# Optimization experiments

Measured on AMD Instinct MI355X. Metric: run time of the kernel, lower is better.

Reference implementation:

```python
import jax, jax.numpy as jnp
import numpy as np

B, L, D_IN, D, P, NL = 8, 4096, 64, 512, 512, 3
EPS = 1e-5


def _ln(x, w, b):
    m = x.mean(-1, keepdims=True)
    v = ((x - m) ** 2).mean(-1, keepdims=True)
    return (x - m) * jax.lax.rsqrt(v + EPS) * w + b


def _gelu(x):
    return jax.nn.gelu(x, approximate=False)  # torch default = exact erf GELU


def _s5_scan(u, lam_re, lam_im, Bre, Bim, Cre, Cim, Dp, log_step):
    # u: (L, D). Diagonal complex SSM with ZOH discretization.
    lam = lam_re + 1j * lam_im                      # (P,)
    step = jnp.exp(log_step)                        # (P,)
    lam_bar = jnp.exp(lam * step)                   # (P,)
    Bt = Bre + 1j * Bim                             # (P, D)
    B_bar = ((lam_bar - 1.0) / lam)[:, None] * Bt   # (P, D)
    Bu = u.astype(jnp.complex64) @ B_bar.T          # (L, P)
    A = jnp.broadcast_to(lam_bar, Bu.shape)         # (L, P)

    def binop(a, b):
        A1, b1 = a
        A2, b2 = b
        return (A2 * A1, A2 * b1 + b2)

    _, xs = jax.lax.associative_scan(binop, (A, Bu))  # (L, P) states
    Ct = Cre + 1j * Cim                               # (D, P)
    return 2.0 * jnp.real(xs @ Ct.T) + Dp * u          # (L, D)


def setup_inputs() -> dict:
    key = jax.random.key(0)
    ks = iter(jax.random.split(key, 32))
    r = lambda s, sc=1.0: sc * jax.random.normal(next(ks), s, dtype=jnp.float32)
    inp = {}
    inp['x'] = r((B, L, D_IN))
    inp['lengths'] = jax.random.randint(next(ks), (B,), 1, L + 1, dtype=jnp.int32)
    inp['enc_w'] = r((D_IN, D), 0.05)
    inp['enc_b'] = jnp.zeros((D,), jnp.float32)
    # S5 SSM params per layer (stacked over NL)
    inp['lam_re'] = -jnp.exp(r((NL, P), 0.5))          # stable: Re(Lambda) < 0
    inp['lam_im'] = np.pi * r((NL, P))
    inp['Bre'] = r((NL, P, D), 1.0 / np.sqrt(D))
    inp['Bim'] = r((NL, P, D), 1.0 / np.sqrt(D))
    inp['Cre'] = r((NL, D, P), 1.0 / np.sqrt(P))
    inp['Cim'] = r((NL, D, P), 1.0 / np.sqrt(P))
    inp['Dp'] = r((NL, D))
    inp['log_step'] = jax.random.uniform(next(ks), (NL, P), jnp.float32, np.log(1e-3), np.log(1e-1))
    # S5Block norms and GEGLU FFN (ff_enc: D->2D no bias, ff_dec: D->D no bias)
    inp['an_w'] = jnp.ones((NL, D), jnp.float32)
    inp['an_b'] = jnp.zeros((NL, D), jnp.float32)
    inp['fn_w'] = jnp.ones((NL, D), jnp.float32)
    inp['fn_b'] = jnp.zeros((NL, D), jnp.float32)
    inp['ffe_w'] = r((NL, 2 * D, D), 1.0 / np.sqrt(D))
    inp['ffd_w'] = r((NL, D, D), 1.0 / np.sqrt(D))
    # outer prenorm LayerNorms
    inp['norm_w'] = jnp.ones((NL, D), jnp.float32)
    inp['norm_b'] = jnp.zeros((NL, D), jnp.float32)
    inp['head_w'] = r((1, D), 0.05)
    inp['head_b'] = jnp.zeros((1,), jnp.float32)
    return inp


def reference(x, lengths, enc_w, enc_b, lam_re, lam_im, Bre, Bim, Cre, Cim, Dp,
              log_step, an_w, an_b, fn_w, fn_b, ffe_w, ffd_w, norm_w, norm_b,
              head_w, head_b):
    h = x @ enc_w + enc_b  # (B, L, D)
    s5_b = jax.vmap(_s5_scan, in_axes=(0, None, None, None, None, None, None, None, None))
    for i in range(NL):
        z = _ln(h, norm_w[i], norm_b[i])  # prenorm (dropout = identity in eval)
        # --- S5Block ---
        fx = _ln(z, an_w[i], an_b[i])
        z = _gelu(s5_b(fx, lam_re[i], lam_im[i], Bre[i], Bim[i], Cre[i], Cim[i], Dp[i], log_step[i])) + fx
        fx = _ln(z, fn_w[i], fn_b[i])
        e = fx @ ffe_w[i].T                      # (B, L, 2D)
        a, g = jnp.split(e, 2, axis=-1)
        z = (a * _gelu(g)) @ ffd_w[i].T + fx      # GEGLU + residual
        h = h + z
    mask = (jnp.arange(L)[None, :] < lengths[:, None])[..., None]  # (B, L, 1)
    pooled = (h * mask).sum(axis=1) / jnp.maximum(lengths, 1)[:, None].astype(h.dtype)
    return (pooled @ head_w.T + head_b).squeeze(-1)  # (B,)
```

## Files before the change

kernel.cpp:

```cpp
#include <hip/hip_runtime.h>
#include <hip/hip_bf16.h>
#include <stdint.h>

#define BB 8
#define LL 4096
#define D_IN 64
#define DD 512
#define PP 512
#define NL 3
#define MTOK (BB * LL)
#define SCHUNK 64
#define SCHUNK_LOG 6
#define NCHUNK (LL / SCHUNK)
#define NCHUNK_LOG 6

typedef __bf16 bf16x8 __attribute__((ext_vector_type(8)));
typedef __bf16 bf16x4 __attribute__((ext_vector_type(4)));
typedef float f32x4 __attribute__((ext_vector_type(4)));

typedef const __attribute__((address_space(1))) void gvoid_t;
typedef __attribute__((address_space(3))) void svoid_t;

__device__ __forceinline__ void async16(const __bf16* g, __bf16* l) {
    __builtin_amdgcn_global_load_lds((gvoid_t*)g, (svoid_t*)l, 16, 0, 0);
}

__device__ __forceinline__ float gelu_f(float x) {
    return 0.5f * x * (1.0f + erff(x * 0.70710678118654752440f));
}
__device__ __forceinline__ float wred(float v) {
#pragma unroll
    for (int o = 32; o > 0; o >>= 1) v += __shfl_xor(v, o, 64);
    return v;
}
__device__ __forceinline__ float bflo(uint32_t u) { return __builtin_bit_cast(float, (uint32_t)(u << 16)); }
__device__ __forceinline__ float bfhi(uint32_t u) { return __builtin_bit_cast(float, (uint32_t)(u & 0xffff0000u)); }
__device__ __forceinline__ uint32_t packbf2(float a, float b) {
    unsigned short ha = __builtin_bit_cast(unsigned short, (__bf16)a);
    unsigned short hb = __builtin_bit_cast(unsigned short, (__bf16)b);
    return (uint32_t)ha | ((uint32_t)hb << 16);
}
__device__ __forceinline__ float ldf(const void* p, long i, int f) {
    return f ? ((const float*)p)[i] : (float)((const __bf16*)p)[i];
}
__device__ __forceinline__ void split1(float v, __bf16& h, __bf16& l) {
    h = (__bf16)v;
    l = (__bf16)(v - (float)h);
}

__global__ void detect(const uint32_t* __restrict__ an_w_raw, int* __restrict__ flag) {
    if (threadIdx.x == 0) *flag = (an_w_raw[0] == 0x3F800000u) ? 1 : 0;
}

template <bool AL, bool BL>
__device__ __forceinline__ void gemm_kloop(
    const __bf16* __restrict__ Ah, const __bf16* __restrict__ Al,
    const __bf16* __restrict__ Bh, const __bf16* __restrict__ Bl,
    long ga, long gb, int lda, int K,
    __bf16* dAh, __bf16* dAl, __bf16* dBh, __bf16* dBl,
    const __bf16* sAh, const __bf16* sAl, const __bf16* sBh, const __bf16* sBl,
    int wm, int wn, int fr, int co, f32x4 (&acc)[4][4])
{
    constexpr int HB = 16384;

    auto stage = [&](int boff, int k0) {
        async16(Ah + ga + k0, dAh + boff);
        async16(Ah + ga + k0 + 16 * (long)lda, dAh + boff + 512);
        if constexpr (AL) {
            async16(Al + ga + k0, dAl + boff);
            async16(Al + ga + k0 + 16 * (long)lda, dAl + boff + 512);
        }
        async16(Bh + gb + k0, dBh + boff);
        async16(Bh + gb + k0 + 16 * (long)K, dBh + boff + 512);
        if constexpr (BL) {
            async16(Bl + gb + k0, dBl + boff);
            async16(Bl + gb + k0 + 16 * (long)K, dBl + boff + 512);
        }
    };

    stage(0, 0);
    asm volatile("s_waitcnt vmcnt(0)" ::: "memory");
    __builtin_amdgcn_s_barrier();
    __builtin_amdgcn_sched_barrier(0);

    int roff = 0;
    for (int k0 = 0; k0 < K; k0 += 32) {
        if (k0 + 32 < K) stage(roff ^ HB, k0 + 32);

        bf16x8 afh[4], afl[4], bfh[4], bfl[4];
#pragma unroll
        for (int i = 0; i < 4; i++) {
            afh[i] = *(const bf16x8*)(sAh + roff + (wm * 64 + i * 16 + fr) * 32 + co);
            bfh[i] = *(const bf16x8*)(sBh + roff + (wn * 64 + i * 16 + fr) * 32 + co);
            if constexpr (AL) afl[i] = *(const bf16x8*)(sAl + roff + (wm * 64 + i * 16 + fr) * 32 + co);
            if constexpr (BL) bfl[i] = *(const bf16x8*)(sBl + roff + (wn * 64 + i * 16 + fr) * 32 + co);
        }
#pragma unroll
        for (int i = 0; i < 4; i++)
#pragma unroll
            for (int j = 0; j < 4; j++) {
                if constexpr (BL)
                    acc[i][j] = __builtin_amdgcn_mfma_f32_16x16x32_bf16(afh[i], bfl[j], acc[i][j], 0, 0, 0);
                if constexpr (AL)
                    acc[i][j] = __builtin_amdgcn_mfma_f32_16x16x32_bf16(afl[i], bfh[j], acc[i][j], 0, 0, 0);
                acc[i][j] = __builtin_amdgcn_mfma_f32_16x16x32_bf16(afh[i], bfh[j], acc[i][j], 0, 0, 0);
            }

        asm volatile("s_waitcnt vmcnt(0) lgkmcnt(0)" ::: "memory");
        __builtin_amdgcn_s_barrier();
        __builtin_amdgcn_sched_barrier(0);
        roff ^= HB;
    }
}

template <int MODE, bool ARAW, bool BRAW>
__global__ __launch_bounds__(256) void gemm_bt(
    const __bf16* __restrict__ Ah, const __bf16* __restrict__ Al, int lda,
    const __bf16* __restrict__ Bh, const __bf16* __restrict__ Bl,
    int M, int N, int K,
    __bf16* outh, __bf16* outl, float* h32,
    __bf16* fxh, __bf16* fxl, const float* __restrict__ vec,
    const int* __restrict__ lengths, float* __restrict__ partials, int b0,
    const int* __restrict__ flag)
{
    __shared__ __attribute__((aligned(16))) char smem[65536];
    __bf16* sAh = (__bf16*)smem;
    __bf16* sAl = (__bf16*)(smem + 8192);
    __bf16* sBh = (__bf16*)(smem + 16384);
    __bf16* sBl = (__bf16*)(smem + 24576);

    const int tid = threadIdx.x;
    const int lane = tid & 63;
    const int wave = tid >> 6;
    const int wm = wave & 1, wn = wave >> 1;
    const long m0 = (long)blockIdx.x * 128;
    const long n0 = (long)blockIdx.y * 128;

    f32x4 acc[4][4] = {};

    const int sr = lane >> 2;
    const int sc = ((lane & 3) ^ ((sr >> 1) & 3)) * 8;
    const long ga = (m0 + wave * 32 + sr) * (long)lda + sc;
    const long gb = (n0 + wave * 32 + sr) * (long)K + sc;
    __bf16* dAh = sAh + wave * 1024;
    __bf16* dAl = sAl + wave * 1024;
    __bf16* dBh = sBh + wave * 1024;
    __bf16* dBl = sBl + wave * 1024;

    const int fr = lane & 15;
    const int co = ((lane >> 4) ^ ((fr >> 1) & 3)) * 8;

    if constexpr (!ARAW && !BRAW) {
        gemm_kloop<true, true>(Ah, Al, Bh, Bl, ga, gb, lda, K, dAh, dAl, dBh, dBl,
                               sAh, sAl, sBh, sBl, wm, wn, fr, co, acc);
    } else {
        const int f32ds = *flag;
        if (f32ds) {
            gemm_kloop<true, true>(Ah, Al, Bh, Bl, ga, gb, lda, K, dAh, dAl, dBh, dBl,
                                   sAh, sAl, sBh, sBl, wm, wn, fr, co, acc);
        } else if constexpr (ARAW && BRAW) {
            gemm_kloop<false, false>(Ah, Al, Bh, Bl, ga, gb, lda, K, dAh, dAl, dBh, dBl,
                                     sAh, sAl, sBh, sBl, wm, wn, fr, co, acc);
        } else if constexpr (!ARAW && BRAW) {
            gemm_kloop<true, false>(Ah, Al, Bh, Bl, ga, gb, lda, K, dAh, dAl, dBh, dBl,
                                    sAh, sAl, sBh, sBl, wm, wn, fr, co, acc);
        } else {
            gemm_kloop<false, true>(Ah, Al, Bh, Bl, ga, gb, lda, K, dAh, dAl, dBh, dBl,
                                    sAh, sAl, sBh, sBl, wm, wn, fr, co, acc);
        }
    }

    float* scratch = (float*)smem + wave * 1088;
    const int er = (lane >> 4) * 4;
    const int ec = lane & 15;
    const int lr_rd = lane >> 3;
    const int lc_rd = (lane & 7) * 8;

    float pacc = 0.f;
    int lenb = 0;
    if (MODE == 5) lenb = lengths[b0 + (int)(blockIdx.x >> 5)];

#pragma unroll
    for (int i = 0; i < 4; i++) {
#pragma unroll
        for (int j = 0; j < 4; j++)
#pragma unroll
            for (int r = 0; r < 4; r++)
                scratch[(er + r) * 68 + j * 16 + ec] = acc[i][j][r];
#pragma unroll
        for (int s = 0; s < 2; s++) {
            const int lr = s * 8 + lr_rd;
            float v8[8];
            *(f32x4*)v8       = *(const f32x4*)&scratch[lr * 68 + lc_rd];
            *(f32x4*)(v8 + 4) = *(const f32x4*)&scratch[lr * 68 + lc_rd + 4];
            const long gm = m0 + wm * 64 + i * 16 + lr;
            const int gc = (int)n0 + wn * 64 + lc_rd;
            if (MODE == 0) {
                const long idx = gm * N + gc;
                bf16x8 h8, l8;
#pragma unroll
                for (int e = 0; e < 8; e++) { __bf16 h, l; split1(v8[e], h, l); h8[e] = h; l8[e] = l; }
                *(bf16x8*)(outh + idx) = h8;
                *(bf16x8*)(outl + idx) = l8;
            } else if (MODE == 1) {
                const long idx = gm * N + gc;
                f32x4 o0, o1;
#pragma unroll
                for (int e = 0; e < 4; e++) { o0[e] = v8[e] + vec[gc + e]; o1[e] = v8[4 + e] + vec[gc + 4 + e]; }
                *(f32x4*)(h32 + idx) = o0;
                *(f32x4*)(h32 + idx + 4) = o1;
            } else if (MODE == 2) {
                const long idx = gm * N + gc;
                const bf16x8 uh = *(const bf16x8*)(fxh + idx);
                const bf16x8 ul = *(const bf16x8*)(fxl + idx);
                bf16x8 h8, l8;
#pragma unroll
                for (int e = 0; e < 8; e++) {
                    const float u = (float)uh[e] + (float)ul[e];
                    const float z = gelu_f(v8[e] + vec[gc + e] * u) + u;
                    __bf16 h, l; split1(z, h, l); h8[e] = h; l8[e] = l;
                }
                *(bf16x8*)(fxh + idx) = h8;
                *(bf16x8*)(fxl + idx) = l8;
            } else if (MODE == 3 || MODE == 5) {
                const long idx = gm * N + gc;
                const bf16x8 uh = *(const bf16x8*)(fxh + idx);
                const bf16x8 ul = *(const bf16x8*)(fxl + idx);
                f32x4 o0 = *(const f32x4*)(h32 + idx);
                f32x4 o1 = *(const f32x4*)(h32 + idx + 4);
#pragma unroll
                for (int e = 0; e < 4; e++) {
                    o0[e] += v8[e] + (float)uh[e] + (float)ul[e];
                    o1[e] += v8[4 + e] + (float)uh[4 + e] + (float)ul[4 + e];
                }
                if (MODE == 3) {
                    *(f32x4*)(h32 + idx) = o0;
                    *(f32x4*)(h32 + idx + 4) = o1;
                } else {
                    if ((int)(gm & (LL - 1)) < lenb) {
#pragma unroll
                        for (int e = 0; e < 4; e++)
                            pacc += o0[e] * vec[gc + e] + o1[e] * vec[gc + 4 + e];
                    }
                }
            } else {
                const long tidx = gm * (N / 2) + (gc >> 1);
                bf16x4 h4, l4;
#pragma unroll
                for (int q = 0; q < 4; q++) {
                    const float t = v8[2 * q] * gelu_f(v8[2 * q + 1]);
                    __bf16 h, l; split1(t, h, l); h4[q] = h; l4[q] = l;
                }
                *(bf16x4*)(outh + tidx) = h4;
                *(bf16x4*)(outl + tidx) = l4;
            }
        }
    }

    if (MODE == 5) {
        pacc = wred(pacc);
        float* red = (float*)(smem + 17408);
        if (lane == 0) red[wave] = pacc;
        __syncthreads();
        if (tid == 0)
            partials[(long)(b0 + (int)(blockIdx.x >> 5)) * 128 +
                     (int)(blockIdx.x & 31) * 4 + (int)blockIdx.y] =
                red[0] + red[1] + red[2] + red[3];
    }
}

template <bool DBL, bool F32IN>
__global__ __launch_bounds__(256) void ln_kernel(
    const float* __restrict__ xf, const __bf16* xh, const __bf16* xl,
    __bf16* oh, __bf16* ol,
    const float* __restrict__ w1, const float* __restrict__ b1,
    const float* __restrict__ w2, const float* __restrict__ b2)
{
    const int lane = threadIdx.x & 63;
    const int wave = threadIdx.x >> 6;
    const long row = (long)blockIdx.x * 4 + wave;
    const int c0 = lane * 8;

    float v[8];
    if (F32IN) {
        const float* xp = xf + row * DD + c0;
        const float4 a = *(const float4*)xp;
        const float4 b = *(const float4*)(xp + 4);
        v[0] = a.x; v[1] = a.y; v[2] = a.z; v[3] = a.w;
        v[4] = b.x; v[5] = b.y; v[6] = b.z; v[7] = b.w;
    } else {
        const bf16x8 a = *(const bf16x8*)(xh + row * DD + c0);
        const bf16x8 b = *(const bf16x8*)(xl + row * DD + c0);
#pragma unroll
        for (int j = 0; j < 8; j++) v[j] = (float)a[j] + (float)b[j];
    }

    float s = 0.f;
#pragma unroll
    for (int j = 0; j < 8; j++) s += v[j];
    s = wred(s);
    float m = s * (1.0f / DD);
    float q = 0.f;
#pragma unroll
    for (int j = 0; j < 8; j++) { const float d = v[j] - m; q += d * d; }
    q = wred(q);
    float rstd = rsqrtf(q * (1.0f / DD) + 1e-5f);
    float y[8];
#pragma unroll
    for (int j = 0; j < 8; j++)
        y[j] = (v[j] - m) * rstd * w1[c0 + j] + b1[c0 + j];

    if (DBL) {
        s = 0.f;
#pragma unroll
        for (int j = 0; j < 8; j++) s += y[j];
        s = wred(s);
        m = s * (1.0f / DD);
        q = 0.f;
#pragma unroll
        for (int j = 0; j < 8; j++) { const float d = y[j] - m; q += d * d; }
        q = wred(q);
        rstd = rsqrtf(q * (1.0f / DD) + 1e-5f);
#pragma unroll
        for (int j = 0; j < 8; j++)
            y[j] = (y[j] - m) * rstd * w2[c0 + j] + b2[c0 + j];
    }

    bf16x8 oh8, ol8;
#pragma unroll
    for (int j = 0; j < 8; j++) { __bf16 h, l; split1(y[j], h, l); oh8[j] = h; ol8[j] = l; }
    *(bf16x8*)(oh + row * DD + c0) = oh8;
    *(bf16x8*)(ol + row * DD + c0) = ol8;
}

__global__ void prep_small(const void* enc_w, __bf16* __restrict__ eh, __bf16* __restrict__ el,
                           const void* lam_re, const void* lam_im, const void* logst,
                           float2* __restrict__ lamb, float2* __restrict__ abars,
                           float2* __restrict__ coef,
                           const void* nw, const void* nb, const void* aw, const void* ab,
                           const void* fw, const void* fb, const void* dp,
                           const void* eb, const void* hw, const void* hb,
                           float* __restrict__ cv, const int* __restrict__ flag)
{
    const int idx = blockIdx.x * 256 + threadIdx.x;
    const int f = *flag;
    {
        const int n = idx >> 6, k = idx & 63;
        __bf16 h, l;
        split1(ldf(enc_w, (long)k * DD + n, f), h, l);
        eh[idx] = h; el[idx] = l;
    }
    if (idx < NL * PP) {
        const float lre = ldf(lam_re, idx, f), lim = ldf(lam_im, idx, f);
        const float st = expf(ldf(logst, idx, f));
        const float ea = expf(lre * st);
        const float ang = lim * st;
        const float br = ea * cosf(ang), bi = ea * sinf(ang);
        lamb[idx] = make_float2(br, bi);
        float ar = br, ai = bi;
#pragma unroll
        for (int q = 0; q < SCHUNK_LOG; q++) { const float t = ar * ar - ai * ai; ai = 2.f * ar * ai; ar = t; }
        abars[idx] = make_float2(ar, ai);
        const float nr = br - 1.f, ni = bi;
        const float den = lre * lre + lim * lim;
        coef[idx] = make_float2((nr * lre + ni * lim) / den, (ni * lre - nr * lim) / den);
    }
    const int NV = NL * DD;
    if (idx < 7 * NV + 1025) {
        if (idx < NV) cv[idx] = ldf(nw, idx, f);
        else if (idx < 2 * NV) cv[idx] = ldf(nb, idx - NV, f);
        else if (idx < 3 * NV) cv[idx] = ldf(aw, idx - 2 * NV, f);
        else if (idx < 4 * NV) cv[idx] = ldf(ab, idx - 3 * NV, f);
        else if (idx < 5 * NV) cv[idx] = ldf(fw, idx - 4 * NV, f);
        else if (idx < 6 * NV) cv[idx] = ldf(fb, idx - 5 * NV, f);
        else if (idx < 7 * NV) cv[idx] = ldf(dp, idx - 6 * NV, f);
        else if (idx < 7 * NV + 512) cv[idx] = ldf(eb, idx - 7 * NV, f);
        else if (idx < 7 * NV + 1024) cv[idx] = ldf(hw, idx - 7 * NV - 512, f);
        else cv[idx] = ldf(hb, idx - 7 * NV - 1024, f);
    }
}

__global__ void prep_w12(const void* Bre, const void* Bim, const float2* __restrict__ coef,
                         __bf16* __restrict__ W1th, __bf16* __restrict__ W1tl,
                         const void* Cre, const void* Cim,
                         __bf16* __restrict__ W2th, __bf16* __restrict__ W2tl,
                         const int* __restrict__ flag)
{
    const long idx = (long)blockIdx.x * 256 + threadIdx.x;
    const int f = *flag;
    const long li = idx >> 18;
    const int pd = (int)(idx & ((1 << 18) - 1));
    {
        const int p = pd >> 9, d = pd & 511;
        const float2 c = coef[li * PP + p];
        const float br = ldf(Bre, idx, f), bi = ldf(Bim, idx, f);
        const float re = c.x * br - c.y * bi;
        const float im = c.x * bi + c.y * br;
        const long base = li * (2 * PP) * DD;
        __bf16 h, l;
        split1(re, h, l); W1th[base + (long)(2 * p) * DD + d] = h; W1tl[base + (long)(2 * p) * DD + d] = l;
        split1(im, h, l); W1th[base + (long)(2 * p + 1) * DD + d] = h; W1tl[base + (long)(2 * p + 1) * DD + d] = l;
    }
    {
        const int d = pd >> 9, p = pd & 511;
        const long base = li * DD * (2 * PP);
        __bf16 h, l;
        split1(2.f * ldf(Cre, idx, f), h, l);
        W2th[base + (long)d * (2 * PP) + 2 * p] = h; W2tl[base + (long)d * (2 * PP) + 2 * p] = l;
        split1(-2.f * ldf(Cim, idx, f), h, l);
        W2th[base + (long)d * (2 * PP) + 2 * p + 1] = h; W2tl[base + (long)d * (2 * PP) + 2 * p + 1] = l;
    }
}

__global__ void prep_ff(const void* ffe, __bf16* __restrict__ feh, __bf16* __restrict__ fel,
                        const void* ffd, __bf16* __restrict__ fdh, __bf16* __restrict__ fdl,
                        const int* __restrict__ flag)
{
    const long idx = (long)blockIdx.x * 256 + threadIdx.x;
    const int f = *flag;
    {
        const long li = idx >> 19;
        const int rc = (int)(idx & ((1 << 19) - 1));
        const int r = rc >> 9, c = rc & 511;
        const int nr = (r < 512) ? (2 * r) : (2 * (r - 512) + 1);
        __bf16 h, l;
        split1(ldf(ffe, idx, f), h, l);
        const long dst = li * (1 << 19) + (long)nr * 512 + c;
        feh[dst] = h; fel[dst] = l;
    }
    if (idx < (long)NL * DD * DD) {
        __bf16 h, l;
        split1(ldf(ffd, idx, f), h, l);
        fdh[idx] = h; fdl[idx] = l;
    }
}

__global__ void split_arr(const void* src, __bf16* __restrict__ dh, __bf16* __restrict__ dl,
                          long n, const int* __restrict__ flag)
{
    const long idx = (long)blockIdx.x * 256 + threadIdx.x;
    if (idx >= n) return;
    __bf16 h, l;
    split1(ldf(src, idx, *flag), h, l);
    dh[idx] = h; dl[idx] = l;
}

__global__ __launch_bounds__(256) void scan_ends(const uint32_t* __restrict__ wh32,
                                                 const uint32_t* __restrict__ wl32,
                                                 const float2* __restrict__ lamb,
                                                 float2* __restrict__ ends)
{
    const int idx = blockIdx.x * 256 + threadIdx.x;
    const int p = idx & 511;
    const int c = (idx >> 9) & (NCHUNK - 1);
    const int b = idx >> (9 + NCHUNK_LOG);
    const float2 lb = lamb[p];
    const long base = ((long)(b * LL + c * SCHUNK)) * 512 + p;
    float sr = 0.f, si = 0.f;
    for (int j = 0; j < SCHUNK; j++) {
        const uint32_t uh = wh32[base + (long)j * 512];
        const uint32_t ul = wl32[base + (long)j * 512];
        const float br = bflo(uh) + bflo(ul);
        const float bi = bfhi(uh) + bfhi(ul);
        const float ns = fmaf(lb.x, sr, fmaf(-lb.y, si, br));
        si = fmaf(lb.x, si, fmaf(lb.y, sr, bi));
        sr = ns;
    }
    ends[((long)b * NCHUNK + c) * PP + p] = make_float2(sr, si);
}

__global__ __launch_bounds__(256) void scan_fix(uint32_t* wh32, uint32_t* wl32,
                                                const float2* __restrict__ lamb,
                                                const float2* __restrict__ abars,
                                                const float2* __restrict__ ends)
{
    const int idx = blockIdx.x * 256 + threadIdx.x;
    const int p = idx & 511;
    const int c = (idx >> 9) & (NCHUNK - 1);
    const int b = idx >> (9 + NCHUNK_LOG);
    const float2 lb = lamb[p];

    const float2 As = abars[p];
    const float2* eb = ends + (long)b * NCHUNK * PP + p;
    float cr = 0.f, ci = 0.f;
    for (int cc = 0; cc < c; cc++) {
        const float2 e = eb[(long)cc * PP];
        const float nr = fmaf(As.x, cr, fmaf(-As.y, ci, e.x));
        ci = fmaf(As.x, ci, fmaf(As.y, cr, e.y));
        cr = nr;
    }

    const long base = ((long)(b * LL + c * SCHUNK)) * 512 + p;
    float sr = cr, si = ci;
    for (int j = 0; j < SCHUNK; j++) {
        const uint32_t uh = wh32[base + (long)j * 512];
        const uint32_t ul = wl32[base + (long)j * 512];
        const float br = bflo(uh) + bflo(ul);
        const float bi = bfhi(uh) + bfhi(ul);
        const float ns = fmaf(lb.x, sr, fmaf(-lb.y, si, br));
        si = fmaf(lb.x, si, fmaf(lb.y, sr, bi));
        sr = ns;
        const float hr = (float)(__bf16)sr, hi_ = (float)(__bf16)si;
        wh32[base + (long)j * 512] = packbf2(sr, si);
        wl32[base + (long)j * 512] = packbf2(sr - hr, si - hi_);
    }
}

__global__ void pool2(const float* __restrict__ partials, const int* __restrict__ lengths,
                      const float* __restrict__ hb_, void* out, const int* __restrict__ flag)
{
    const int b = threadIdx.x;
    if (b >= BB) return;
    float s = 0.f;
    for (int c = 0; c < 128; c++) s += partials[b * 128 + c];
    const int len = lengths[b] < 1 ? 1 : lengths[b];
    const float val = s / (float)len + hb_[0];
    if (*flag) ((float*)out)[b] = val;
    else ((__bf16*)out)[b] = (__bf16)val;
}

extern "C" void kernel_launch(void* const* d_in, const int* in_sizes, int n_in,
                              void* d_out, int out_size, void* d_ws, size_t ws_size,
                              hipStream_t stream)
{
    const void* x      = d_in[0];
    const int* lengths = (const int*)d_in[1];
    const void* enc_w  = d_in[2];
    const void* enc_b  = d_in[3];
    const void* lam_re = d_in[4];
    const void* lam_im = d_in[5];
    const void* Bre    = d_in[6];
    const void* Bim    = d_in[7];
    const void* Cre    = d_in[8];
    const void* Cim    = d_in[9];
    const void* Dp     = d_in[10];
    const void* logst  = d_in[11];
    const void* an_w   = d_in[12];
    const void* an_b   = d_in[13];
    const void* fn_w   = d_in[14];
    const void* fn_b   = d_in[15];
    const void* ffe    = d_in[16];
    const void* ffd    = d_in[17];
    const void* norm_w = d_in[18];
    const void* norm_b = d_in[19];
    const void* head_w = d_in[20];
    const void* head_b = d_in[21];

    char* w = (char*)d_ws;
    auto alloc = [&](size_t bytes) -> char* {
        char* r = w;
        w += (bytes + 255) & ~(size_t)255;
        return r;
    };
    int* dflag    = (int*)alloc(256);
    __bf16* W1th  = (__bf16*)alloc((size_t)NL * 2 * PP * DD * 2);
    __bf16* W1tl  = (__bf16*)alloc((size_t)NL * 2 * PP * DD * 2);
    __bf16* W2th  = (__bf16*)alloc((size_t)NL * DD * 2 * PP * 2);
    __bf16* W2tl  = (__bf16*)alloc((size_t)NL * DD * 2 * PP * 2);
    __bf16* ffeh  = (__bf16*)alloc((size_t)NL * 2 * DD * DD * 2);
    __bf16* ffel  = (__bf16*)alloc((size_t)NL * 2 * DD * DD * 2);
    __bf16* ffdh  = (__bf16*)alloc((size_t)NL * DD * DD * 2);
    __bf16* ffdl  = (__bf16*)alloc((size_t)NL * DD * DD * 2);
    __bf16* ench  = (__bf16*)alloc((size_t)DD * D_IN * 2);
    __bf16* encl  = (__bf16*)alloc((size_t)DD * D_IN * 2);
    __bf16* xh    = (__bf16*)alloc((size_t)MTOK * D_IN * 2);
    __bf16* xl    = (__bf16*)alloc((size_t)MTOK * D_IN * 2);
    float2* lamb  = (float2*)alloc((size_t)NL * PP * 8);
    float2* abars = (float2*)alloc((size_t)NL * PP * 8);
    float2* coef  = (float2*)alloc((size_t)NL * PP * 8);
    float*  cv    = (float*)alloc((size_t)(7 * NL * DD + 1025) * 4);
    float2* ends  = (float2*)alloc((size_t)BB * PP * NCHUNK * 8);
    float* partials = (float*)alloc((size_t)BB * 128 * 4);
    const size_t fixed = (size_t)(w - (char*)d_ws);

    int NB = BB;
    const size_t per_b = (size_t)LL * DD * 16;
    while (NB > 1 && fixed + (size_t)NB * per_b > ws_size) NB >>= 1;
    float* h32  = (float*)alloc((size_t)NB * LL * DD * 4);
    __bf16* fxh = (__bf16*)alloc((size_t)NB * LL * DD * 2);
    __bf16* fxl = (__bf16*)alloc((size_t)NB * LL * DD * 2);
    __bf16* wh  = (__bf16*)alloc((size_t)NB * LL * 2 * PP * 2);
    __bf16* wl  = (__bf16*)alloc((size_t)NB * LL * 2 * PP * 2);

    const float* cv_nw = cv;
    const float* cv_nb = cv + 1536;
    const float* cv_aw = cv + 3072;
    const float* cv_ab = cv + 4608;
    const float* cv_fw = cv + 6144;
    const float* cv_fb = cv + 7680;
    const float* cv_dp = cv + 9216;
    const float* cv_eb = cv + 10752;
    const float* cv_hw = cv + 11264;
    const float* cv_hb = cv + 11776;

    detect<<<1, 64, 0, stream>>>((const uint32_t*)an_w, dflag);
    prep_small<<<128, 256, 0, stream>>>(enc_w, ench, encl, lam_re, lam_im, logst,
                                        lamb, abars, coef,
                                        norm_w, norm_b, an_w, an_b, fn_w, fn_b, Dp,
                                        enc_b, head_w, head_b, cv, dflag);
    prep_w12<<<(NL * PP * DD) / 256, 256, 0, stream>>>(
        Bre, Bim, coef, W1th, W1tl, Cre, Cim, W2th, W2tl, dflag);
    prep_ff<<<((size_t)NL * 2 * DD * DD) / 256, 256, 0, stream>>>(
        ffe, ffeh, ffel, ffd, ffdh, ffdl, dflag);
    split_arr<<<((size_t)MTOK * D_IN + 255) / 256, 256, 0, stream>>>(
        x, xh, xl, (long)MTOK * D_IN, dflag);

    for (int b0 = 0; b0 < BB; b0 += NB) {
        const int M = NB * LL;
        gemm_bt<1, true, true><<<dim3(M / 128, DD / 128), 256, 0, stream>>>(
            xh + (long)b0 * LL * D_IN, xl + (long)b0 * LL * D_IN, D_IN,
            ench, encl, M, DD, D_IN, nullptr, nullptr, h32, nullptr, nullptr, cv_eb,
            nullptr, nullptr, 0, dflag);

        for (int li = 0; li < NL; li++) {
            ln_kernel<true, true><<<M / 4, 256, 0, stream>>>(
                h32, nullptr, nullptr, fxh, fxl,
                cv_nw + li * DD, cv_nb + li * DD, cv_aw + li * DD, cv_ab + li * DD);
            gemm_bt<0, false, false><<<dim3(M / 128, (2 * PP) / 128), 256, 0, stream>>>(
                fxh, fxl, DD, W1th + (long)li * 2 * PP * DD, W1tl + (long)li * 2 * PP * DD,
                M, 2 * PP, DD, wh, wl, nullptr, nullptr, nullptr, nullptr,
                nullptr, nullptr, 0, dflag);
            scan_ends<<<(NB * NCHUNK * PP) / 256, 256, 0, stream>>>(
                (const uint32_t*)wh, (const uint32_t*)wl, lamb + li * PP, ends);
            scan_fix<<<(NB * NCHUNK * PP) / 256, 256, 0, stream>>>(
                (uint32_t*)wh, (uint32_t*)wl, lamb + li * PP, abars + li * PP, ends);
            gemm_bt<2, false, true><<<dim3(M / 128, DD / 128), 256, 0, stream>>>(
                wh, wl, 2 * PP, W2th + (long)li * DD * 2 * PP, W2tl + (long)li * DD * 2 * PP,
                M, DD, 2 * PP, nullptr, nullptr, nullptr, fxh, fxl, cv_dp + li * DD,
                nullptr, nullptr, 0, dflag);
            ln_kernel<false, false><<<M / 4, 256, 0, stream>>>(
                nullptr, fxh, fxl, fxh, fxl,
                cv_fw + li * DD, cv_fb + li * DD, nullptr, nullptr);
            gemm_bt<4, false, true><<<dim3(M / 128, (2 * DD) / 128), 256, 0, stream>>>(
                fxh, fxl, DD, ffeh + (long)li * 2 * DD * DD, ffel + (long)li * 2 * DD * DD,
                M, 2 * DD, DD, wh, wl, nullptr, nullptr, nullptr, nullptr,
                nullptr, nullptr, 0, dflag);
            if (li < NL - 1) {
                gemm_bt<3, false, true><<<dim3(M / 128, DD / 128), 256, 0, stream>>>(
                    wh, wl, DD, ffdh + (long)li * DD * DD, ffdl + (long)li * DD * DD,
                    M, DD, DD, nullptr, nullptr, h32, fxh, fxl, nullptr,
                    nullptr, nullptr, 0, dflag);
            } else {
                gemm_bt<5, false, true><<<dim3(M / 128, DD / 128), 256, 0, stream>>>(
                    wh, wl, DD, ffdh + (long)li * DD * DD, ffdl + (long)li * DD * DD,
                    M, DD, DD, nullptr, nullptr, h32, fxh, fxl, cv_hw,
                    lengths, partials, b0, dflag);
            }
        }
    }
    pool2<<<1, 64, 0, stream>>>(partials, lengths, cv_hb, d_out, dflag);
}
```

Before: 1.846 ms.

## Fuse chunk-end scan state computation into the B-projection GEMM epilogue

Drops the separate scan_ends kernel. The first SSM GEMM's epilogue now builds per-chunk scan end states from its own register outputs: each lane runs a short recurrence over its 8 rows, then the lanes combine their partial states with precomputed powers of lambda_bar through xor shuffles. Lambda powers 0..8 are added to prep_small. This saves one full read of the complex Bu tensor and one launch per layer, at the cost of extra epilogue arithmetic, register pressure, and a changed floating-point summation order.

Result: no change. 1.816 ms (-1.6%).

```diff
diff --git a/kernel.cpp b/kernel.cpp
--- a/kernel.cpp
+++ b/kernel.cpp
@@ -120,6 +120,7 @@
     int M, int N, int K,
     __bf16* outh, __bf16* outl, float* h32,
     __bf16* fxh, __bf16* fxl, const float* __restrict__ vec,
+    const float2* __restrict__ lamp, float2* __restrict__ endsw,
     const int* __restrict__ lengths, float* __restrict__ partials, int b0,
     const int* __restrict__ flag)
 {
@@ -180,6 +181,19 @@
     int lenb = 0;
     if (MODE == 5) lenb = lengths[b0 + (int)(blockIdx.x >> 5)];
 
+    float st_re[4], st_im[4];
+    float c8r[4], c8i[4], csr[4], csi[4];
+    if constexpr (MODE == 0) {
+        const int p0 = ((int)n0 + wn * 64 + lc_rd) >> 1;
+#pragma unroll
+        for (int q = 0; q < 4; q++) {
+            st_re[q] = 0.f; st_im[q] = 0.f;
+            const float2 l8 = lamp[(p0 + q) * 9 + 8];
+            const float2 ls = lamp[(p0 + q) * 9 + (7 - lr_rd)];
+            c8r[q] = l8.x; c8i[q] = l8.y; csr[q] = ls.x; csi[q] = ls.y;
+        }
+    }
+
 #pragma unroll
     for (int i = 0; i < 4; i++) {
 #pragma unroll
@@ -202,6 +216,14 @@
                 for (int e = 0; e < 8; e++) { __bf16 h, l; split1(v8[e], h, l); h8[e] = h; l8[e] = l; }
                 *(bf16x8*)(outh + idx) = h8;
                 *(bf16x8*)(outl + idx) = l8;
+#pragma unroll
+                for (int q = 0; q < 4; q++) {
+                    const float ur = (float)h8[2 * q] + (float)l8[2 * q];
+                    const float ui = (float)h8[2 * q + 1] + (float)l8[2 * q + 1];
+                    const float nr = fmaf(c8r[q], st_re[q], fmaf(-c8i[q], st_im[q], ur));
+                    st_im[q] = fmaf(c8r[q], st_im[q], fmaf(c8i[q], st_re[q], ui));
+                    st_re[q] = nr;
+                }
             } else if (MODE == 1) {
                 const long idx = gm * N + gc;
                 f32x4 o0, o1;
@@ -257,6 +279,28 @@
         }
     }
 
+    if constexpr (MODE == 0) {
+#pragma unroll
+        for (int q = 0; q < 4; q++) {
+            float er2 = csr[q] * st_re[q] - csi[q] * st_im[q];
+            float ei2 = csr[q] * st_im[q] + csi[q] * st_re[q];
+#pragma unroll
+            for (int o = 8; o <= 32; o <<= 1) {
+                er2 += __shfl_xor(er2, o, 64);
+                ei2 += __shfl_xor(ei2, o, 64);
+            }
+            st_re[q] = er2; st_im[q] = ei2;
+        }
+        if (lr_rd == 0) {
+            const int b = (int)(m0 >> 12);
+            const int c = (int)((m0 & (LL - 1)) >> 6) + wm;
+            const int p0 = ((int)n0 + wn * 64 + lc_rd) >> 1;
+            float2* ep = endsw + ((long)b * NCHUNK + c) * PP + p0;
+#pragma unroll
+            for (int q = 0; q < 4; q++) ep[q] = make_float2(st_re[q], st_im[q]);
+        }
+    }
+
     if (MODE == 5) {
         pacc = wred(pacc);
         float* red = (float*)(smem + 17408);
@@ -336,7 +380,7 @@
 __global__ void prep_small(const void* enc_w, __bf16* __restrict__ eh, __bf16* __restrict__ el,
                            const void* lam_re, const void* lam_im, const void* logst,
                            float2* __restrict__ lamb, float2* __restrict__ abars,
-                           float2* __restrict__ coef,
+                           float2* __restrict__ coef, float2* __restrict__ lampows,
                            const void* nw, const void* nb, const void* aw, const void* ab,
                            const void* fw, const void* fb, const void* dp,
                            const void* eb, const void* hw, const void* hb,
@@ -364,6 +408,14 @@
         const float nr = br - 1.f, ni = bi;
         const float den = lre * lre + lim * lim;
         coef[idx] = make_float2((nr * lre + ni * lim) / den, (ni * lre - nr * lim) / den);
+        float pr = 1.f, pi = 0.f;
+#pragma unroll
+        for (int e = 0; e <= 8; e++) {
+            lampows[(long)idx * 9 + e] = make_float2(pr, pi);
+            const float t = pr * br - pi * bi;
+            pi = pr * bi + pi * br;
+            pr = t;
+        }
     }
     const int NV = NL * DD;
     if (idx < 7 * NV + 1025) {
@@ -443,30 +495,6 @@
     __bf16 h, l;
     split1(ldf(src, idx, *flag), h, l);
     dh[idx] = h; dl[idx] = l;
-}
-
-__global__ __launch_bounds__(256) void scan_ends(const uint32_t* __restrict__ wh32,
-                                                 const uint32_t* __restrict__ wl32,
-                                                 const float2* __restrict__ lamb,
-                                                 float2* __restrict__ ends)
-{
-    const int idx = blockIdx.x * 256 + threadIdx.x;
-    const int p = idx & 511;
-    const int c = (idx >> 9) & (NCHUNK - 1);
-    const int b = idx >> (9 + NCHUNK_LOG);
-    const float2 lb = lamb[p];
-    const long base = ((long)(b * LL + c * SCHUNK)) * 512 + p;
-    float sr = 0.f, si = 0.f;
-    for (int j = 0; j < SCHUNK; j++) {
-        const uint32_t uh = wh32[base + (long)j * 512];
-        const uint32_t ul = wl32[base + (long)j * 512];
-        const float br = bflo(uh) + bflo(ul);
-        const float bi = bfhi(uh) + bfhi(ul);
-        const float ns = fmaf(lb.x, sr, fmaf(-lb.y, si, br));
-        si = fmaf(lb.x, si, fmaf(lb.y, sr, bi));
-        sr = ns;
-    }
-    ends[((long)b * NCHUNK + c) * PP + p] = make_float2(sr, si);
 }
 
 __global__ __launch_bounds__(256) void scan_fix(uint32_t* wh32, uint32_t* wl32,
@@ -568,6 +596,7 @@
     float2* lamb  = (float2*)alloc((size_t)NL * PP * 8);
     float2* abars = (float2*)alloc((size_t)NL * PP * 8);
     float2* coef  = (float2*)alloc((size_t)NL * PP * 8);
+    float2* lampows = (float2*)alloc((size_t)NL * PP * 9 * 8);
     float*  cv    = (float*)alloc((size_t)(7 * NL * DD + 1025) * 4);
     float2* ends  = (float2*)alloc((size_t)BB * PP * NCHUNK * 8);
     float* partials = (float*)alloc((size_t)BB * 128 * 4);
@@ -595,7 +624,7 @@
 
     detect<<<1, 64, 0, stream>>>((const uint32_t*)an_w, dflag);
     prep_small<<<128, 256, 0, stream>>>(enc_w, ench, encl, lam_re, lam_im, logst,
-                                        lamb, abars, coef,
+                                        lamb, abars, coef, lampows,
                                         norm_w, norm_b, an_w, an_b, fn_w, fn_b, Dp,
                                         enc_b, head_w, head_b, cv, dflag);
     prep_w12<<<(NL * PP * DD) / 256, 256, 0, stream>>>(
@@ -610,7 +639,7 @@
         gemm_bt<1, true, true><<<dim3(M / 128, DD / 128), 256, 0, stream>>>(
             xh + (long)b0 * LL * D_IN, xl + (long)b0 * LL * D_IN, D_IN,
             ench, encl, M, DD, D_IN, nullptr, nullptr, h32, nullptr, nullptr, cv_eb,
-            nullptr, nullptr, 0, dflag);
+            nullptr, nullptr, nullptr, nullptr, 0, dflag);
 
         for (int li = 0; li < NL; li++) {
             ln_kernel<true, true><<<M / 4, 256, 0, stream>>>(
@@ -619,32 +648,31 @@
             gemm_bt<0, false, false><<<dim3(M / 128, (2 * PP) / 128), 256, 0, stream>>>(
                 fxh, fxl, DD, W1th + (long)li * 2 * PP * DD, W1tl + (long)li * 2 * PP * DD,
                 M, 2 * PP, DD, wh, wl, nullptr, nullptr, nullptr, nullptr,
+                lampows + (long)li * PP * 9, ends,
                 nullptr, nullptr, 0, dflag);
-            scan_ends<<<(NB * NCHUNK * PP) / 256, 256, 0, stream>>>(
-                (const uint32_t*)wh, (const uint32_t*)wl, lamb + li * PP, ends);
             scan_fix<<<(NB * NCHUNK * PP) / 256, 256, 0, stream>>>(
                 (uint32_t*)wh, (uint32_t*)wl, lamb + li * PP, abars + li * PP, ends);
             gemm_bt<2, false, true><<<dim3(M / 128, DD / 128), 256, 0, stream>>>(
                 wh, wl, 2 * PP, W2th + (long)li * DD * 2 * PP, W2tl + (long)li * DD * 2 * PP,
                 M, DD, 2 * PP, nullptr, nullptr, nullptr, fxh, fxl, cv_dp + li * DD,
-                nullptr, nullptr, 0, dflag);
+                nullptr, nullptr, nullptr, nullptr, 0, dflag);
             ln_kernel<false, false><<<M / 4, 256, 0, stream>>>(
                 nullptr, fxh, fxl, fxh, fxl,
                 cv_fw + li * DD, cv_fb + li * DD, nullptr, nullptr);
             gemm_bt<4, false, true><<<dim3(M / 128, (2 * DD) / 128), 256, 0, stream>>>(
                 fxh, fxl, DD, ffeh + (long)li * 2 * DD * DD, ffel + (long)li * 2 * DD * DD,
                 M, 2 * DD, DD, wh, wl, nullptr, nullptr, nullptr, nullptr,
-                nullptr, nullptr, 0, dflag);
+                nullptr, nullptr, nullptr, nullptr, 0, dflag);
             if (li < NL - 1) {
                 gemm_bt<3, false, true><<<dim3(M / 128, DD / 128), 256, 0, stream>>>(
                     wh, wl, DD, ffdh + (long)li * DD * DD, ffdl + (long)li * DD * DD,
                     M, DD, DD, nullptr, nullptr, h32, fxh, fxl, nullptr,
-                    nullptr, nullptr, 0, dflag);
+                    nullptr, nullptr, nullptr, nullptr, 0, dflag);
             } else {
                 gemm_bt<5, false, true><<<dim3(M / 128, DD / 128), 256, 0, stream>>>(
                     wh, wl, DD, ffdh + (long)li * DD * DD, ffdl + (long)li * DD * DD,
                     M, DD, DD, nullptr, nullptr, h32, fxh, fxl, cv_hw,
-                    lengths, partials, b0, dflag);
+                    nullptr, nullptr, lengths, partials, b0, dflag);
             }
         }
     }
```
